# Optimization experiments

Hardware: AMD Instinct MI355X
Metric: run time of the kernel (lower is better)

## Reference

```python
import jax, jax.numpy as jnp
import numpy as np

B, S, D = 4, 2048, 512


def _dyt(x, alpha, w, b):
    return jnp.tanh(alpha * x) * w + b


def _fourier_fourier_attn(x, qr, qi, kr, ki, vr, vi, rtr, rti):
    xc = x.astype(jnp.complex64)
    qw, kw, vw, rtw = qr + 1j * qi, kr + 1j * ki, vr + 1j * vi, rtr + 1j * rti
    Xf = jnp.fft.fft(xc, axis=-1)  # [B,S,D] complex
    q = jnp.fft.fft(Xf * qw, axis=-2)
    k = jnp.fft.fft(Xf * kw, axis=-2)
    v = jnp.fft.fft(Xf * vw, axis=-2)
    rt = q / (k + 1e-12) * v
    rt = jnp.fft.ifft(rt, axis=-2) * rtw
    return jnp.fft.ifft(rt, axis=-1).real


def _fourier_sdpa(x, qr, qi, kr, ki, vr, vi):
    xc = x.astype(jnp.complex64)
    Xf = jnp.fft.fft(xc, axis=-1)
    proj = lambda w: jnp.fft.ifft(Xf * w, axis=-1).real
    q = proj(qr + 1j * qi)
    k = proj(kr + 1j * ki)
    v = proj(vr + 1j * vi)
    scores = jnp.einsum('bsd,btd->bst', q, k) / np.sqrt(D).astype(np.float32)
    attn = jax.nn.softmax(scores, axis=-1)
    return jnp.einsum('bst,btd->bsd', attn, v)


def _fourier_ffn(x, ar, ai, br, bi, bias):
    # Faithful to the source: the gelu branch is overwritten (dead code),
    # the returned value only uses the b-weighted FFT path.
    xc = x.astype(jnp.complex64)
    Xf = jnp.fft.fft(xc, axis=-1)
    h = jnp.fft.ifft(Xf * (ar + 1j * ai), axis=-1).real + bias
    h = jax.nn.gelu(h, approximate=False)  # discarded, as in the original
    return jnp.fft.ifft(Xf * (br + 1j * bi), axis=-1).real


def setup_inputs() -> dict:
    key = jax.random.key(0)
    ks = jax.random.split(key, 32)
    d = {'x': jax.random.normal(ks[0], (B, S, D), dtype=jnp.float32)}
    names_real = ['a_qr', 'a_kr', 'a_vr', 'a_rtr', 'b_qr', 'b_kr', 'b_vr', 'f_ar', 'f_br']
    names_imag = ['a_qi', 'a_ki', 'a_vi', 'a_rti', 'b_qi', 'b_ki', 'b_vi', 'f_ai', 'f_bi']
    i = 1
    for n in names_real:
        d[n] = 1.0 + 0.02 * jax.random.normal(ks[i], (D,), dtype=jnp.float32); i += 1
    for n in names_imag:
        d[n] = 0.02 * jax.random.normal(ks[i], (D,), dtype=jnp.float32); i += 1
    d['f_bias'] = 0.02 * jax.random.normal(ks[i], (D,), dtype=jnp.float32); i += 1
    for p in ['dyta', 'dytb', 'dytf']:
        d[p + '_alpha'] = jnp.full((1,), 0.5, dtype=jnp.float32)
        d[p + '_w'] = 1.0 + 0.02 * jax.random.normal(ks[i], (D,), dtype=jnp.float32); i += 1
        d[p + '_b'] = 0.02 * jax.random.normal(ks[i], (D,), dtype=jnp.float32); i += 1
    return d


def reference(x, a_qr, a_qi, a_kr, a_ki, a_vr, a_vi, a_rtr, a_rti,
              dyta_alpha, dyta_w, dyta_b,
              b_qr, b_qi, b_kr, b_ki, b_vr, b_vi,
              dytb_alpha, dytb_w, dytb_b,
              f_ar, f_ai, f_br, f_bi, f_bias,
              dytf_alpha, dytf_w, dytf_b):
    # attn_a block: FourierFourierAttention(DyT(x)) + x
    x = _fourier_fourier_attn(_dyt(x, dyta_alpha, dyta_w, dyta_b),
                              a_qr, a_qi, a_kr, a_ki, a_vr, a_vi, a_rtr, a_rti) + x
    # attn_b block: FourierScaledDotProductAttention(DyT(x)) + x
    x = _fourier_sdpa(_dyt(x, dytb_alpha, dytb_w, dytb_b),
                      b_qr, b_qi, b_kr, b_ki, b_vr, b_vi) + x
    # ffn block: FourierForwardNetwork(DyT(x)) + x
    x = _fourier_ffn(_dyt(x, dytf_alpha, dytf_w, dytf_b),
                     f_ar, f_ai, f_br, f_bi, f_bias) + x
    return x
```

## Files before the change

kernel.cpp:

```cpp
#include <hip/hip_runtime.h>


typedef __attribute__((ext_vector_type(8))) __bf16 bf16x8;
typedef __attribute__((ext_vector_type(4))) float floatx4;
typedef __attribute__((ext_vector_type(8))) _Float16 halfx8;
typedef __attribute__((ext_vector_type(8))) unsigned short ushortx8;
typedef __attribute__((ext_vector_type(2))) _Float16 half2v;
typedef __attribute__((ext_vector_type(4))) _Float16 half4v;

__device__ __forceinline__ unsigned short f2bf(float x) {
    unsigned u = __float_as_uint(x);
    u = (u + 0x7fffu + ((u >> 16) & 1u)) >> 16;
    return (unsigned short)u;
}

__device__ __forceinline__ float dyt_tanh(float x) {
    float e = __expf(2.0f * x);
    return 1.0f - 2.0f / (e + 1.0f);
}

__device__ __forceinline__ void async_load16(const unsigned short* g, unsigned short* l) {
    __builtin_amdgcn_global_load_lds(
        (const __attribute__((address_space(1))) unsigned int*)g,
        (__attribute__((address_space(3))) unsigned int*)l, 16, 0, 0);
}

__device__ __forceinline__ void wtw512(float (&tc)[12], float (&ts)[12], int lane) {
    const float w = -6.28318530717958647692f / 512.0f;
#pragma unroll
    for (int j = 0; j < 4; j++) __sincosf(w * (float)(j * 64 + lane), &ts[j], &tc[j]);
#pragma unroll
    for (int j = 0; j < 2; j++) __sincosf(w * (float)(2 * (j * 64 + lane)), &ts[4 + j], &tc[4 + j]);
    __sincosf(w * (float)(4 * lane), &ts[6], &tc[6]);
    __sincosf(w * (float)(8 * (lane & 31)), &ts[7], &tc[7]);
    __sincosf(w * (float)(16 * (lane & 15)), &ts[8], &tc[8]);
    __sincosf(w * (float)(32 * (lane & 7)), &ts[9], &tc[9]);
    __sincosf(w * (float)(64 * (lane & 3)), &ts[10], &tc[10]);
    __sincosf(w * (float)(128 * (lane & 1)), &ts[11], &tc[11]);
}

template <bool INV>
__device__ __forceinline__ void wfft512(float (&re)[8], float (&im)[8],
                                        const float (&tc)[12], const float (&ts)[12], int lane) {
    if (!INV) {
#pragma unroll
        for (int j = 0; j < 4; j++) {
            float ur = re[j], ui = im[j], vr = re[j + 4], vi = im[j + 4];
            re[j] = ur + vr; im[j] = ui + vi;
            float dr = ur - vr, di = ui - vi;
            re[j + 4] = dr * tc[j] - di * ts[j];
            im[j + 4] = dr * ts[j] + di * tc[j];
        }
#pragma unroll
        for (int g = 0; g < 8; g += 4)
#pragma unroll
            for (int jj = 0; jj < 2; jj++) {
                int j = g + jj;
                float ur = re[j], ui = im[j], vr = re[j + 2], vi = im[j + 2];
                re[j] = ur + vr; im[j] = ui + vi;
                float dr = ur - vr, di = ui - vi;
                re[j + 2] = dr * tc[4 + jj] - di * ts[4 + jj];
                im[j + 2] = dr * ts[4 + jj] + di * tc[4 + jj];
            }
#pragma unroll
        for (int j = 0; j < 8; j += 2) {
            float ur = re[j], ui = im[j], vr = re[j + 1], vi = im[j + 1];
            re[j] = ur + vr; im[j] = ui + vi;
            float dr = ur - vr, di = ui - vi;
            re[j + 1] = dr * tc[6] - di * ts[6];
            im[j + 1] = dr * ts[6] + di * tc[6];
        }
#pragma unroll
        for (int st = 0; st < 6; st++) {
            int h = 32 >> st;
            bool hi = (lane & h) != 0;
            float c = (st < 5) ? tc[7 + st] : 1.0f;
            float s = (st < 5) ? ts[7 + st] : 0.0f;
#pragma unroll
            for (int j = 0; j < 8; j++) {
                float orr = __shfl_xor(re[j], h, 64);
                float oii = __shfl_xor(im[j], h, 64);
                float dr = orr - re[j], di = oii - im[j];
                float sr = re[j] + orr, si = im[j] + oii;
                re[j] = hi ? (dr * c - di * s) : sr;
                im[j] = hi ? (dr * s + di * c) : si;
            }
        }
    } else {
#pragma unroll
        for (int st = 5; st >= 0; st--) {
            int h = 32 >> st;
            bool hi = (lane & h) != 0;
            float c = (st < 5) ? tc[7 + st] : 1.0f;
            float s = (st < 5) ? ts[7 + st] : 0.0f;
#pragma unroll
            for (int j = 0; j < 8; j++) {
                float zr = re[j], zi = im[j];
                float vr = zr * c + zi * s;
                float vi = zi * c - zr * s;
                float mr = hi ? vr : zr;
                float mi = hi ? vi : zi;
                float orr = __shfl_xor(mr, h, 64);
                float oii = __shfl_xor(mi, h, 64);
                re[j] = hi ? (orr - vr) : (zr + orr);
                im[j] = hi ? (oii - vi) : (zi + oii);
            }
        }
#pragma unroll
        for (int j = 0; j < 8; j += 2) {
            float vr = re[j + 1] * tc[6] + im[j + 1] * ts[6];
            float vi = im[j + 1] * tc[6] - re[j + 1] * ts[6];
            re[j + 1] = re[j] - vr; im[j + 1] = im[j] - vi;
            re[j] += vr; im[j] += vi;
        }
#pragma unroll
        for (int g = 0; g < 8; g += 4)
#pragma unroll
            for (int jj = 0; jj < 2; jj++) {
                int j = g + jj;
                float vr = re[j + 2] * tc[4 + jj] + im[j + 2] * ts[4 + jj];
                float vi = im[j + 2] * tc[4 + jj] - re[j + 2] * ts[4 + jj];
                re[j + 2] = re[j] - vr; im[j + 2] = im[j] - vi;
                re[j] += vr; im[j] += vi;
            }
#pragma unroll
        for (int j = 0; j < 4; j++) {
            float vr = re[j + 4] * tc[j] + im[j + 4] * ts[j];
            float vi = im[j + 4] * tc[j] - re[j + 4] * ts[j];
            re[j + 4] = re[j] - vr; im[j + 4] = im[j] - vi;
            re[j] += vr; im[j] += vi;
        }
    }
}

__global__ __launch_bounds__(256, 4) void k1_dyt_fftd(
        const float* __restrict__ x,
        const float* __restrict__ alpha, const float* __restrict__ w, const float* __restrict__ bia,
        half2v* __restrict__ xf) {
    int tid = threadIdx.x, lane = tid & 63, wv = tid >> 6;
    size_t row = (size_t)blockIdx.x * 4 + wv;
    float tc[12], ts[12];
    wtw512(tc, ts, lane);
    float re[8], im[8];
    float a = alpha[0];
    const float* xr = x + row * 512;
#pragma unroll
    for (int j = 0; j < 8; j++) {
        int d = j * 64 + lane;
        re[j] = dyt_tanh(a * xr[d]) * w[d] + bia[d];
        im[j] = 0.f;
    }
    wfft512<false>(re, im, tc, ts, lane);
#pragma unroll
    for (int j = 0; j < 8; j++) {
        int d = j * 64 + lane;
        xf[row * 512 + d] = (half2v){(_Float16)re[j], (_Float16)im[j]};
    }
}

__device__ __forceinline__ int pidx4(int i) { return i + (i >> 3); }

__device__ __forceinline__ void r4_fwd(float4* X, int t, int h, const half2v* tw) {
    int pos = t & (h - 1);
    int i = ((t & ~(h - 1)) << 2) | pos;
    int i0 = pidx4(i), i1 = pidx4(i + h), i2 = pidx4(i + 2 * h), i3 = pidx4(i + 3 * h);
    float4 a0 = X[i0], a1 = X[i1], a2 = X[i2], a3 = X[i3];
    half2v wv = tw[pos];
    float c1 = (float)wv.x, s1 = (float)wv.y;
    float c2 = c1 * c1 - s1 * s1, s2 = 2.f * c1 * s1;
    float c3 = c2 * c1 - s2 * s1, s3 = s2 * c1 + c2 * s1;
    float4 o0, o1, o2, o3;
    {
        float t0r = a0.x + a2.x, t0i = a0.y + a2.y, t1r = a0.x - a2.x, t1i = a0.y - a2.y;
        float t2r = a1.x + a3.x, t2i = a1.y + a3.y, t3r = a1.x - a3.x, t3i = a1.y - a3.y;
        o0.x = t0r + t2r; o0.y = t0i + t2i;
        float b1r = t1r + t3i, b1i = t1i - t3r;
        float b2r = t0r - t2r, b2i = t0i - t2i;
        float b3r = t1r - t3i, b3i = t1i + t3r;
        o1.x = b1r * c1 - b1i * s1; o1.y = b1r * s1 + b1i * c1;
        o2.x = b2r * c2 - b2i * s2; o2.y = b2r * s2 + b2i * c2;
        o3.x = b3r * c3 - b3i * s3; o3.y = b3r * s3 + b3i * c3;
    }
    {
        float t0r = a0.z + a2.z, t0i = a0.w + a2.w, t1r = a0.z - a2.z, t1i = a0.w - a2.w;
        float t2r = a1.z + a3.z, t2i = a1.w + a3.w, t3r = a1.z - a3.z, t3i = a1.w - a3.w;
        o0.z = t0r + t2r; o0.w = t0i + t2i;
        float b1r = t1r + t3i, b1i = t1i - t3r;
        float b2r = t0r - t2r, b2i = t0i - t2i;
        float b3r = t1r - t3i, b3i = t1i + t3r;
        o1.z = b1r * c1 - b1i * s1; o1.w = b1r * s1 + b1i * c1;
        o2.z = b2r * c2 - b2i * s2; o2.w = b2r * s2 + b2i * c2;
        o3.z = b3r * c3 - b3i * s3; o3.w = b3r * s3 + b3i * c3;
    }
    X[i0] = o0; X[i1] = o1; X[i2] = o2; X[i3] = o3;
}

__device__ __forceinline__ void r4_inv(float4* X, int t, int h, const half2v* tw) {
    int pos = t & (h - 1);
    int i = ((t & ~(h - 1)) << 2) | pos;
    int i0 = pidx4(i), i1 = pidx4(i + h), i2 = pidx4(i + 2 * h), i3 = pidx4(i + 3 * h);
    float4 y0 = X[i0], y1 = X[i1], y2 = X[i2], y3 = X[i3];
    half2v wv = tw[pos];
    float c1 = (float)wv.x, s1 = (float)wv.y;
    float c2 = c1 * c1 - s1 * s1, s2 = 2.f * c1 * s1;
    float c3 = c2 * c1 - s2 * s1, s3 = s2 * c1 + c2 * s1;
    float4 o0, o1, o2, o3;
    {
        float u1r = y1.x * c1 + y1.y * s1, u1i = y1.y * c1 - y1.x * s1;
        float u2r = y2.x * c2 + y2.y * s2, u2i = y2.y * c2 - y2.x * s2;
        float u3r = y3.x * c3 + y3.y * s3, u3i = y3.y * c3 - y3.x * s3;
        float s0r = y0.x + u2r, s0i = y0.y + u2i;
        float s1r = y0.x - u2r, s1i = y0.y - u2i;
        float s2r = u1r + u3r, s2i = u1i + u3i;
        float s3r = u1r - u3r, s3i = u1i - u3i;
        o0.x = s0r + s2r; o0.y = s0i + s2i;
        o2.x = s0r - s2r; o2.y = s0i - s2i;
        o1.x = s1r - s3i; o1.y = s1i + s3r;
        o3.x = s1r + s3i; o3.y = s1i - s3r;
    }
    {
        float u1r = y1.z * c1 + y1.w * s1, u1i = y1.w * c1 - y1.z * s1;
        float u2r = y2.z * c2 + y2.w * s2, u2i = y2.w * c2 - y2.z * s2;
        float u3r = y3.z * c3 + y3.w * s3, u3i = y3.w * c3 - y3.z * s3;
        float s0r = y0.z + u2r, s0i = y0.w + u2i;
        float s1r = y0.z - u2r, s1i = y0.w - u2i;
        float s2r = u1r + u3r, s2i = u1i + u3i;
        float s3r = u1r - u3r, s3i = u1i - u3i;
        o0.z = s0r + s2r; o0.w = s0i + s2i;
        o2.z = s0r - s2r; o2.w = s0i - s2i;
        o1.z = s1r - s3i; o1.w = s1i + s3r;
        o3.z = s1r + s3i; o3.w = s1i - s3r;
    }
    X[i0] = o0; X[i1] = o1; X[i2] = o2; X[i3] = o3;
}

__global__ __launch_bounds__(512) void k2_sfft(
        half2v* __restrict__ xf,
        const float* __restrict__ qr, const float* __restrict__ qi,
        const float* __restrict__ kr, const float* __restrict__ ki,
        const float* __restrict__ vr, const float* __restrict__ vi,
        const float* __restrict__ rtr, const float* __restrict__ rti) {
    __shared__ float4 buf[2304];
    __shared__ half2v twd[682];
    int t = threadIdx.x;
    int g = blockIdx.x;
    int xcd = g & 7, r = g >> 3;
    int pp = xcd * 32 + (r & 31);
    int b = r >> 5;
    int p0 = pp * 2;
    half4v* colh = (half4v*)(xf + (size_t)b * 2048 * 512 + p0);

    for (int i = t; i < 682; i += 512) {
        int h, off;
        if (i < 512)      { h = 512; off = 0; }
        else if (i < 640) { h = 128; off = 512; }
        else if (i < 672) { h = 32;  off = 640; }
        else if (i < 680) { h = 8;   off = 672; }
        else              { h = 2;   off = 680; }
        int pos = i - off;
        float s, c;
        __sincosf(-6.28318530717958647692f * (float)pos / (float)(4 * h), &s, &c);
        twd[i] = (half2v){(_Float16)c, (_Float16)s};
    }

#pragma unroll
    for (int c = 0; c < 4; c++) {
        int s = t + 512 * c;
        half4v h = colh[(size_t)s * 256];
        buf[pidx4(s)] = make_float4((float)h.x, (float)h.y, (float)h.z, (float)h.w);
    }
    __syncthreads(); r4_fwd(buf, t, 512, twd);
    __syncthreads(); r4_fwd(buf, t, 128, twd + 512);
    __syncthreads(); r4_fwd(buf, t, 32, twd + 640);
    __syncthreads(); r4_fwd(buf, t, 8, twd + 672);
    __syncthreads(); r4_fwd(buf, t, 2, twd + 680);
    __syncthreads();
#pragma unroll
    for (int c = 0; c < 2; c++) {
        int pr = t + 512 * c;
        int ia = pidx4(2 * pr), ib = pidx4(2 * pr + 1);
        float4 a = buf[ia], bb = buf[ib];
        buf[ia] = make_float4(a.x + bb.x, a.y + bb.y, a.z + bb.z, a.w + bb.w);
        buf[ib] = make_float4(a.x - bb.x, a.y - bb.y, a.z - bb.z, a.w - bb.w);
    }
    __syncthreads();

    int f0 = __brev((unsigned)p0) >> 23;
    int f1 = __brev((unsigned)(p0 + 1)) >> 23;
    float qw0r = qr[f0], qw0i = qi[f0], kw0r = kr[f0], kw0i = ki[f0], vw0r = vr[f0], vw0i = vi[f0];
    float qw1r = qr[f1], qw1i = qi[f1], kw1r = kr[f1], kw1i = ki[f1], vw1r = vr[f1], vw1i = vi[f1];
#pragma unroll
    for (int c = 0; c < 4; c++) {
        int idx = pidx4(t + 512 * c);
        float4 y = buf[idx];
        {
            float yr = y.x, yi = y.y;
            float qre = yr * qw0r - yi * qw0i, qim = yr * qw0i + yi * qw0r;
            float kre = yr * kw0r - yi * kw0i + 1e-12f, kim = yr * kw0i + yi * kw0r;
            float vre = yr * vw0r - yi * vw0i, vim = yr * vw0i + yi * vw0r;
            float inv = 1.0f / (kre * kre + kim * kim);
            float dre = (qre * kre + qim * kim) * inv;
            float dim = (qim * kre - qre * kim) * inv;
            y.x = dre * vre - dim * vim;
            y.y = dre * vim + dim * vre;
        }
        {
            float yr = y.z, yi = y.w;
            float qre = yr * qw1r - yi * qw1i, qim = yr * qw1i + yi * qw1r;
            float kre = yr * kw1r - yi * kw1i + 1e-12f, kim = yr * kw1i + yi * kw1r;
            float vre = yr * vw1r - yi * vw1i, vim = yr * vw1i + yi * vw1r;
            float inv = 1.0f / (kre * kre + kim * kim);
            float dre = (qre * kre + qim * kim) * inv;
            float dim = (qim * kre - qre * kim) * inv;
            y.z = dre * vre - dim * vim;
            y.w = dre * vim + dim * vre;
        }
        buf[idx] = y;
    }

    __syncthreads();
#pragma unroll
    for (int c = 0; c < 2; c++) {
        int pr = t + 512 * c;
        int ia = pidx4(2 * pr), ib = pidx4(2 * pr + 1);
        float4 a = buf[ia], bb = buf[ib];
        buf[ia] = make_float4(a.x + bb.x, a.y + bb.y, a.z + bb.z, a.w + bb.w);
        buf[ib] = make_float4(a.x - bb.x, a.y - bb.y, a.z - bb.z, a.w - bb.w);
    }
    __syncthreads(); r4_inv(buf, t, 2, twd + 680);
    __syncthreads(); r4_inv(buf, t, 8, twd + 672);
    __syncthreads(); r4_inv(buf, t, 32, twd + 640);
    __syncthreads(); r4_inv(buf, t, 128, twd + 512);
    __syncthreads(); r4_inv(buf, t, 512, twd);
    __syncthreads();

    const float sc = 1.0f / 2048.0f;
    float r0r = rtr[f0] * sc, r0i = rti[f0] * sc;
    float r1r = rtr[f1] * sc, r1i = rti[f1] * sc;
#pragma unroll
    for (int c = 0; c < 4; c++) {
        int s = t + 512 * c;
        float4 z = buf[pidx4(s)];
        float ox = z.x * r0r - z.y * r0i, oy = z.x * r0i + z.y * r0r;
        float oz = z.z * r1r - z.w * r1i, ow = z.z * r1i + z.w * r1r;
        colh[(size_t)s * 256] = (half4v){(_Float16)ox, (_Float16)oy, (_Float16)oz, (_Float16)ow};
    }
}

__global__ __launch_bounds__(256, 4) void k3_mid(
        const half2v* __restrict__ xf,
        const float* __restrict__ x,
        const float* __restrict__ alpha, const float* __restrict__ w, const float* __restrict__ bia,
        const float* __restrict__ qr, const float* __restrict__ qi,
        const float* __restrict__ kr, const float* __restrict__ ki,
        const float* __restrict__ vr, const float* __restrict__ vi,
        float* __restrict__ x1,
        unsigned short* __restrict__ qb, unsigned short* __restrict__ kb, unsigned short* __restrict__ vb) {
    __shared__ __align__(16) char smem[4 * 1024 * 8];
    int tid = threadIdx.x, lane = tid & 63, wv = tid >> 6;
    float2* zb = (float2*)(smem + wv * 8192);
    float* wbs = (float*)smem;
    float2* zf = (float2*)(smem + 12288 + wv * 4096);
    size_t pr = (size_t)blockIdx.x * 4 + wv;
    size_t r1 = pr * 2, r2 = r1 + 1;
    float tc[12], ts[12];
    wtw512(tc, ts, lane);

    float xa[8], xb2[8];
#pragma unroll
    for (int j = 0; j < 8; j++) {
        int d = j * 64 + lane;
        half2v h1 = xf[r1 * 512 + d];
        half2v h2 = xf[r2 * 512 + d];
        zb[d]       = make_float2((float)h1.x, (float)h1.y);
        zb[512 + d] = make_float2((float)h2.x, (float)h2.y);
        xa[j]  = x[r1 * 512 + d];
        xb2[j] = x[r2 * 512 + d];
    }
    float re[8], im[8];
#pragma unroll
    for (int j = 0; j < 8; j++) {
        int d = j * 64 + lane;
        int fd = __brev((unsigned)d) >> 23;
        int dp = __brev((unsigned)((512 - fd) & 511)) >> 23;
        float2 z1 = zb[d], z1p = zb[dp];
        float2 z2 = zb[512 + d], z2p = zb[512 + dp];
        float h1r = 0.5f * (z1.x + z1p.x), h1i = 0.5f * (z1.y - z1p.y);
        float h2r = 0.5f * (z2.x + z2p.x), h2i = 0.5f * (z2.y - z2p.y);
        re[j] = h1r - h2i;
        im[j] = h1i + h2r;
    }
    __syncthreads();
    for (int idx = tid; idx < 512; idx += 256) {
        int f = __brev((unsigned)idx) >> 23;
        int gg = (512 - f) & 511;
        float aa = (f == 0 || f == 256) ? 0.04419417382415922f : 0.0625f;
        float ah = aa * 0.5f;
        const float s5 = 0.5f * (1.0f / 512.0f);
        wbs[0 * 512 + idx] = ah * (qr[f] + qr[gg]); wbs[1 * 512 + idx] = ah * (qi[f] - qi[gg]);
        wbs[2 * 512 + idx] = ah * (kr[f] + kr[gg]); wbs[3 * 512 + idx] = ah * (ki[f] - ki[gg]);
        wbs[4 * 512 + idx] = s5 * (vr[f] + vr[gg]); wbs[5 * 512 + idx] = s5 * (vi[f] - vi[gg]);
    }

    wfft512<true>(re, im, tc, ts, lane);
    float a = alpha[0];
    float gre[8], gim[8];
#pragma unroll
    for (int j = 0; j < 8; j++) {
        int d = j * 64 + lane;
        float v1 = re[j] * (1.0f / 512.0f) + xa[j];
        float v2 = im[j] * (1.0f / 512.0f) + xb2[j];
        x1[r1 * 512 + d] = v1;
        x1[r2 * 512 + d] = v2;
        gre[j] = dyt_tanh(a * v1) * w[d] + bia[d];
        gim[j] = dyt_tanh(a * v2) * w[d] + bia[d];
    }
    wfft512<false>(gre, gim, tc, ts, lane);
    __syncthreads();

#pragma unroll
    for (int j = 0; j < 8; j++)
        zf[j * 64 + lane] = make_float2(gre[j], gim[j]);

    float pvr[8], pvi[8];
#pragma unroll
    for (int j = 0; j < 8; j++) {
        int i = j * 64 + lane;
        float wr0 = wbs[4 * 512 + i], wi0 = wbs[5 * 512 + i];
        pvr[j] = gre[j] * wr0 - gim[j] * wi0;
        pvi[j] = gre[j] * wi0 + gim[j] * wr0;
    }

    bool odd = (lane & 1) != 0;
#pragma unroll
    for (int j = 0; j < 8; j++) {
        int d = j * 64 + lane;
        int fd = __brev((unsigned)d) >> 23;
        int dp = __brev((unsigned)((512 - fd) & 511)) >> 23;
        float2 Zp = zf[dp];
        float zr = gre[j], zi = gim[j];
        float A1r = 0.5f * (zr + Zp.x), A1i = 0.5f * (zi - Zp.y);
        float A2r = 0.5f * (zi + Zp.y), A2i = 0.5f * (Zp.x - zr);
        float wr0 = wbs[0 * 512 + d], wi0 = wbs[1 * 512 + d];
        float Q1r = A1r * wr0 - A1i * wi0, Q1i = A1r * wi0 + A1i * wr0;
        float Q2r = A2r * wr0 - A2i * wi0, Q2i = A2r * wi0 + A2i * wr0;
        qb[r1 * 512 + d] = f2bf(odd ? -Q1i : Q1r);
        qb[r2 * 512 + d] = f2bf(odd ? -Q2i : Q2r);
        float wr1 = wbs[2 * 512 + d], wi1 = wbs[3 * 512 + d];
        float K1r = A1r * wr1 - A1i * wi1, K1i = A1r * wi1 + A1i * wr1;
        float K2r = A2r * wr1 - A2i * wi1, K2i = A2r * wi1 + A2i * wr1;
        kb[r1 * 512 + d] = f2bf(odd ? -K1i : K1r);
        kb[r2 * 512 + d] = f2bf(odd ? -K2i : K2r);
    }

    wfft512<true>(pvr, pvi, tc, ts, lane);
#pragma unroll
    for (int j = 0; j < 8; j++) {
        int d = j * 64 + lane;
        vb[r1 * 512 + d] = f2bf(pvr[j]);
        vb[r2 * 512 + d] = f2bf(pvi[j]);
    }
}

__global__ __launch_bounds__(256) void gemm_bt(
        const unsigned short* __restrict__ A, const unsigned short* __restrict__ Bt,
        void* __restrict__ C, int M, int N, int Ks, int kseg, float scale, int out_half) {
    int tilesM = M >> 7, tilesN = N >> 7;
    int perBatch = tilesM * tilesN;
    int l = blockIdx.x;
    int seg = blockIdx.y;
    int s = l & 7, t = l >> 3;
    int cnt = perBatch >> 3;
    int bz = t / cnt;
    int u = t - bz * cnt;
    int pn = tilesN >> 1, pm = tilesM >> 2;
    int n0 = ((s & 1) * pn + (u % pn)) << 7;
    int m0 = ((s >> 1) * pm + (u / pn)) << 7;
    int kbase = seg * kseg;

    const unsigned short* Ab = A + (size_t)bz * M * Ks;
    const unsigned short* Bb = Bt + (size_t)bz * N * Ks;
    __shared__ __align__(16) unsigned short smem[2 * 128 * 64];
    unsigned short* As = smem;
    unsigned short* Bs = smem + 128 * 64;
    int tid = threadIdx.x;
    int wave = tid >> 6, lane = tid & 63;
    int wm = (wave >> 1) * 64, wn = (wave & 1) * 64;
    int lrow = lane & 15, lq = lane >> 4;
    floatx4 acc[4][4];
#pragma unroll
    for (int i = 0; i < 4; i++)
#pragma unroll
        for (int j = 0; j < 4; j++)
            acc[i][j] = (floatx4){0.f, 0.f, 0.f, 0.f};

    int lr = lane >> 3;
    int lcs = lane & 7;
    for (int k0 = kbase; k0 < kbase + kseg; k0 += 64) {
        __syncthreads();
#pragma unroll
        for (int i = 0; i < 4; i++) {
            int c = wave * 4 + i;
            int r = c * 8 + lr;
            int gcol = ((lcs ^ (r & 7)) << 3);
            async_load16(Ab + (size_t)(m0 + r) * Ks + k0 + gcol, As + c * 512);
            async_load16(Bb + (size_t)(n0 + r) * Ks + k0 + gcol, Bs + c * 512);
        }
        __syncthreads();
        bf16x8 a0[4], a1[4], b0[4], b1[4];
#pragma unroll
        for (int mi = 0; mi < 4; mi++) {
            int r = wm + mi * 16 + lrow;
            a0[mi] = *(const bf16x8*)(As + r * 64 + ((lq ^ (r & 7)) << 3));
            a1[mi] = *(const bf16x8*)(As + r * 64 + (((lq + 4) ^ (r & 7)) << 3));
        }
#pragma unroll
        for (int ni = 0; ni < 4; ni++) {
            int r = wn + ni * 16 + lrow;
            b0[ni] = *(const bf16x8*)(Bs + r * 64 + ((lq ^ (r & 7)) << 3));
            b1[ni] = *(const bf16x8*)(Bs + r * 64 + (((lq + 4) ^ (r & 7)) << 3));
        }
#pragma unroll
        for (int mi = 0; mi < 4; mi++)
#pragma unroll
            for (int ni = 0; ni < 4; ni++) {
                acc[mi][ni] = __builtin_amdgcn_mfma_f32_16x16x32_bf16(a0[mi], b0[ni], acc[mi][ni], 0, 0, 0);
                acc[mi][ni] = __builtin_amdgcn_mfma_f32_16x16x32_bf16(a1[mi], b1[ni], acc[mi][ni], 0, 0, 0);
            }
    }
    size_t cbase = ((size_t)seg * 4 + bz) * (size_t)M * N;
    int lr0 = (wave >> 1) * 16 + lq * 4;
    for (int mi = 0; mi < 4; mi++) {
        __syncthreads();
        if (out_half) {
            _Float16* Cs = (_Float16*)smem;
            for (int ni = 0; ni < 4; ni++)
                for (int r = 0; r < 4; r++)
                    Cs[(lr0 + r) * 128 + wn + ni * 16 + lrow] = (_Float16)(acc[mi][ni][r] * scale);
            __syncthreads();
            for (int h = 0; h < 2; h++) {
                int chunk = tid + h * 256;
                int rl = chunk >> 4, cb = (chunk & 15) * 16;
                int grow = m0 + mi * 16 + (rl & 15) + (rl >> 4) * 64;
                *(uint4*)((char*)C + (cbase + (size_t)grow * N + n0) * 2 + cb) =
                    *(const uint4*)((const char*)Cs + rl * 256 + cb);
            }
        } else {
            float* Cs = (float*)smem;
            for (int ni = 0; ni < 4; ni++)
                for (int r = 0; r < 4; r++)
                    Cs[(lr0 + r) * 128 + wn + ni * 16 + lrow] = acc[mi][ni][r] * scale;
            __syncthreads();
            for (int h = 0; h < 4; h++) {
                int chunk = tid + h * 256;
                int rl = chunk >> 5, cb = (chunk & 31) * 16;
                int grow = m0 + mi * 16 + (rl & 15) + (rl >> 4) * 64;
                *(uint4*)((char*)C + (cbase + (size_t)grow * N + n0) * 4 + cb) =
                    *(const uint4*)((const char*)Cs + rl * 512 + cb);
            }
        }
    }
}

__global__ __launch_bounds__(256) void sm_tr(
        const _Float16* __restrict__ Sc, unsigned short* __restrict__ P,
        const unsigned short* __restrict__ vb, unsigned short* __restrict__ vT) {
    __shared__ __align__(16) char lds[64 * 65 * 2];
    if (blockIdx.x < 8192) {
        float* red = (float*)lds;
        int tid = threadIdx.x;
        size_t row = blockIdx.x;
        halfx8 hv = *(const halfx8*)(Sc + row * 2048 + tid * 8);
        float v[8];
#pragma unroll
        for (int j = 0; j < 8; j++) v[j] = (float)hv[j];
        float mx = v[0];
#pragma unroll
        for (int j = 1; j < 8; j++) mx = fmaxf(mx, v[j]);
        for (int off = 32; off >= 1; off >>= 1) mx = fmaxf(mx, __shfl_xor(mx, off));
        int wv = tid >> 6;
        if ((tid & 63) == 0) red[wv] = mx;
        __syncthreads();
        mx = fmaxf(fmaxf(red[0], red[1]), fmaxf(red[2], red[3]));
        float e[8], sum = 0.f;
#pragma unroll
        for (int j = 0; j < 8; j++) { e[j] = __expf(v[j] - mx); sum += e[j]; }
        for (int off = 32; off >= 1; off >>= 1) sum += __shfl_xor(sum, off);
        __syncthreads();
        if ((tid & 63) == 0) red[wv] = sum;
        __syncthreads();
        float inv = 1.0f / (red[0] + red[1] + red[2] + red[3]);
        ushortx8 o;
#pragma unroll
        for (int j = 0; j < 8; j++) o[j] = f2bf(e[j] * inv);
        *(ushortx8*)(P + row * 2048 + tid * 8) = o;
    } else {
        unsigned short (*tile)[65] = (unsigned short (*)[65])lds;
        int id = blockIdx.x - 8192;
        int sx = id & 31, dy = (id >> 5) & 7, bz = id >> 8;
        int s0 = sx * 64, d0 = dy * 64;
        int tx = threadIdx.x & 63, ty = threadIdx.x >> 6;
        for (int j = 0; j < 16; j++) {
            int s = ty + j * 4;
            tile[s][tx] = vb[((size_t)bz * 2048 + s0 + s) * 512 + d0 + tx];
        }
        __syncthreads();
        for (int j = 0; j < 16; j++) {
            int d = ty + j * 4;
            vT[((size_t)bz * 512 + d0 + d) * 2048 + s0 + tx] = tile[tx][d];
        }
    }
}

__global__ __launch_bounds__(256, 4) void k5_ffn(
        const _Float16* __restrict__ attn0, const _Float16* __restrict__ attn1,
        const float* __restrict__ x1,
        const float* __restrict__ alpha, const float* __restrict__ w, const float* __restrict__ bia,
        const float* __restrict__ br, const float* __restrict__ bi,
        float* __restrict__ out) {
    __shared__ float wbs[2][512];
    int tid = threadIdx.x, lane = tid & 63, wv = tid >> 6;
    size_t pr = (size_t)blockIdx.x * 4 + wv;
    size_t r1 = pr * 2, r2 = r1 + 1;
    for (int idx = tid; idx < 512; idx += 256) {
        int f = __brev((unsigned)idx) >> 23;
        int gg = (512 - f) & 511;
        wbs[0][idx] = 0.5f * (br[f] + br[gg]) * (1.0f / 512.0f);
        wbs[1][idx] = 0.5f * (bi[f] - bi[gg]) * (1.0f / 512.0f);
    }
    float tc[12], ts[12];
    wtw512(tc, ts, lane);
    float a = alpha[0];
    float re[8], im[8], x2a[8], x2b[8];
#pragma unroll
    for (int j = 0; j < 8; j++) {
        int d = j * 64 + lane;
        float v1 = (float)attn0[r1 * 512 + d] + (float)attn1[r1 * 512 + d] + x1[r1 * 512 + d];
        float v2 = (float)attn0[r2 * 512 + d] + (float)attn1[r2 * 512 + d] + x1[r2 * 512 + d];
        x2a[j] = v1; x2b[j] = v2;
        re[j] = dyt_tanh(a * v1) * w[d] + bia[d];
        im[j] = dyt_tanh(a * v2) * w[d] + bia[d];
    }
    wfft512<false>(re, im, tc, ts, lane);
    __syncthreads();
#pragma unroll
    for (int j = 0; j < 8; j++) {
        int i = j * 64 + lane;
        float wr0 = wbs[0][i], wi0 = wbs[1][i];
        float rr = re[j], ii = im[j];
        re[j] = rr * wr0 - ii * wi0;
        im[j] = rr * wi0 + ii * wr0;
    }
    wfft512<true>(re, im, tc, ts, lane);
#pragma unroll
    for (int j = 0; j < 8; j++) {
        int d = j * 64 + lane;
        out[r1 * 512 + d] = re[j] + x2a[j];
        out[r2 * 512 + d] = im[j] + x2b[j];
    }
}

extern "C" void kernel_launch(void* const* d_in, const int* in_sizes, int n_in,
                              void* d_out, int out_size, void* d_ws, size_t ws_size,
                              hipStream_t stream) {
    const float* x      = (const float*)d_in[0];
    const float* a_qr   = (const float*)d_in[1];
    const float* a_kr   = (const float*)d_in[2];
    const float* a_vr   = (const float*)d_in[3];
    const float* a_rtr  = (const float*)d_in[4];
    const float* b_qr   = (const float*)d_in[5];
    const float* b_kr   = (const float*)d_in[6];
    const float* b_vr   = (const float*)d_in[7];
    const float* f_br   = (const float*)d_in[9];
    const float* a_qi   = (const float*)d_in[10];
    const float* a_ki   = (const float*)d_in[11];
    const float* a_vi   = (const float*)d_in[12];
    const float* a_rti  = (const float*)d_in[13];
    const float* b_qi   = (const float*)d_in[14];
    const float* b_ki   = (const float*)d_in[15];
    const float* b_vi   = (const float*)d_in[16];
    const float* f_bi   = (const float*)d_in[18];
    const float* dyta_alpha = (const float*)d_in[20];
    const float* dyta_w     = (const float*)d_in[21];
    const float* dyta_b     = (const float*)d_in[22];
    const float* dytb_alpha = (const float*)d_in[23];
    const float* dytb_w     = (const float*)d_in[24];
    const float* dytb_b     = (const float*)d_in[25];
    const float* dytf_alpha = (const float*)d_in[26];
    const float* dytf_w     = (const float*)d_in[27];
    const float* dytf_b     = (const float*)d_in[28];
    (void)in_sizes; (void)n_in; (void)out_size; (void)ws_size;

    char* ws = (char*)d_ws;
    const size_t MB = 1024 * 1024;
    half2v* xfH = (half2v*)(ws + 0 * MB);
    float* x1   = (float*)(ws + 32 * MB);
    unsigned short* qb = (unsigned short*)(ws + 48 * MB);
    unsigned short* kb = (unsigned short*)(ws + 56 * MB);
    unsigned short* vb = (unsigned short*)(ws + 64 * MB);
    unsigned short* vT = (unsigned short*)(ws + 72 * MB);
    _Float16* scores   = (_Float16*)(ws + 0 * MB);
    unsigned short* Pb = (unsigned short*)(ws + 0 * MB);
    _Float16* attnP    = (_Float16*)(ws + 81 * MB);
    float* outp = (float*)d_out;

    k1_dyt_fftd<<<2048, 256, 0, stream>>>(x, dyta_alpha, dyta_w, dyta_b, xfH);
    k2_sfft<<<1024, 512, 0, stream>>>(xfH, a_qr, a_qi, a_kr, a_ki, a_vr, a_vi, a_rtr, a_rti);
    k3_mid<<<1024, 256, 0, stream>>>(xfH, x, dytb_alpha, dytb_w, dytb_b,
                                     b_qr, b_qi, b_kr, b_ki, b_vr, b_vi, x1, qb, kb, vb);
    gemm_bt<<<1024, 256, 0, stream>>>(qb, kb, scores, 2048, 2048, 512, 512,
                                      0.04419417382415922f, 1);
    sm_tr<<<9216, 256, 0, stream>>>(scores, Pb, vb, vT);
    gemm_bt<<<dim3(256, 2), 256, 0, stream>>>(Pb, vT, attnP, 2048, 512, 2048, 1024,
                                              1.0f, 1);
    k5_ffn<<<1024, 256, 0, stream>>>(attnP, attnP + (size_t)4 * 2048 * 512, x1,
                                     dytf_alpha, dytf_w, dytf_b, f_br, f_bi, outp);
}
```

Baseline: 279.9 us.

## Process four rows per wave in k3_mid with a dual interleaved FFT

```diff
diff --git a/kernel.cpp b/kernel.cpp
--- a/kernel.cpp
+++ b/kernel.cpp
@@ -129,6 +129,171 @@
             float vi = im[j + 4] * tc[j] - re[j + 4] * ts[j];
             re[j + 4] = re[j] - vr; im[j + 4] = im[j] - vi;
             re[j] += vr; im[j] += vi;
+        }
+    }
+}
+
+template <bool INV>
+__device__ __forceinline__ void wfft512d(float (&reA)[8], float (&imA)[8],
+                                         float (&reB)[8], float (&imB)[8],
+                                         const float (&tc)[12], const float (&ts)[12], int lane) {
+    if (!INV) {
+#pragma unroll
+        for (int j = 0; j < 4; j++) {
+            {
+                float ur = reA[j], ui = imA[j], vr = reA[j + 4], vi = imA[j + 4];
+                reA[j] = ur + vr; imA[j] = ui + vi;
+                float dr = ur - vr, di = ui - vi;
+                reA[j + 4] = dr * tc[j] - di * ts[j];
+                imA[j + 4] = dr * ts[j] + di * tc[j];
+            }
+            {
+                float ur = reB[j], ui = imB[j], vr = reB[j + 4], vi = imB[j + 4];
+                reB[j] = ur + vr; imB[j] = ui + vi;
+                float dr = ur - vr, di = ui - vi;
+                reB[j + 4] = dr * tc[j] - di * ts[j];
+                imB[j + 4] = dr * ts[j] + di * tc[j];
+            }
+        }
+#pragma unroll
+        for (int g = 0; g < 8; g += 4)
+#pragma unroll
+            for (int jj = 0; jj < 2; jj++) {
+                int j = g + jj;
+                {
+                    float ur = reA[j], ui = imA[j], vr = reA[j + 2], vi = imA[j + 2];
+                    reA[j] = ur + vr; imA[j] = ui + vi;
+                    float dr = ur - vr, di = ui - vi;
+                    reA[j + 2] = dr * tc[4 + jj] - di * ts[4 + jj];
+                    imA[j + 2] = dr * ts[4 + jj] + di * tc[4 + jj];
+                }
+                {
+                    float ur = reB[j], ui = imB[j], vr = reB[j + 2], vi = imB[j + 2];
+                    reB[j] = ur + vr; imB[j] = ui + vi;
+                    float dr = ur - vr, di = ui - vi;
+                    reB[j + 2] = dr * tc[4 + jj] - di * ts[4 + jj];
+                    imB[j + 2] = dr * ts[4 + jj] + di * tc[4 + jj];
+                }
+            }
+#pragma unroll
+        for (int j = 0; j < 8; j += 2) {
+            {
+                float ur = reA[j], ui = imA[j], vr = reA[j + 1], vi = imA[j + 1];
+                reA[j] = ur + vr; imA[j] = ui + vi;
+                float dr = ur - vr, di = ui - vi;
+                reA[j + 1] = dr * tc[6] - di * ts[6];
+                imA[j + 1] = dr * ts[6] + di * tc[6];
+            }
+            {
+                float ur = reB[j], ui = imB[j], vr = reB[j + 1], vi = imB[j + 1];
+                reB[j] = ur + vr; imB[j] = ui + vi;
+                float dr = ur - vr, di = ui - vi;
+                reB[j + 1] = dr * tc[6] - di * ts[6];
+                imB[j + 1] = dr * ts[6] + di * tc[6];
+            }
+        }
+#pragma unroll
+        for (int st = 0; st < 6; st++) {
+            int h = 32 >> st;
+            bool hi = (lane & h) != 0;
+            float c = (st < 5) ? tc[7 + st] : 1.0f;
+            float s = (st < 5) ? ts[7 + st] : 0.0f;
+#pragma unroll
+            for (int j = 0; j < 8; j++) {
+                float oAr = __shfl_xor(reA[j], h, 64);
+                float oAi = __shfl_xor(imA[j], h, 64);
+                float oBr = __shfl_xor(reB[j], h, 64);
+                float oBi = __shfl_xor(imB[j], h, 64);
+                {
+                    float dr = oAr - reA[j], di = oAi - imA[j];
+                    float sr = reA[j] + oAr, si = imA[j] + oAi;
+                    reA[j] = hi ? (dr * c - di * s) : sr;
+                    imA[j] = hi ? (dr * s + di * c) : si;
+                }
+                {
+                    float dr = oBr - reB[j], di = oBi - imB[j];
+                    float sr = reB[j] + oBr, si = imB[j] + oBi;
+                    reB[j] = hi ? (dr * c - di * s) : sr;
+                    imB[j] = hi ? (dr * s + di * c) : si;
+                }
+            }
+        }
+    } else {
+#pragma unroll
+        for (int st = 5; st >= 0; st--) {
+            int h = 32 >> st;
+            bool hi = (lane & h) != 0;
+            float c = (st < 5) ? tc[7 + st] : 1.0f;
+            float s = (st < 5) ? ts[7 + st] : 0.0f;
+#pragma unroll
+            for (int j = 0; j < 8; j++) {
+                float zAr = reA[j], zAi = imA[j];
+                float vAr = zAr * c + zAi * s;
+                float vAi = zAi * c - zAr * s;
+                float mAr = hi ? vAr : zAr;
+                float mAi = hi ? vAi : zAi;
+                float zBr = reB[j], zBi = imB[j];
+                float vBr = zBr * c + zBi * s;
+                float vBi = zBi * c - zBr * s;
+                float mBr = hi ? vBr : zBr;
+                float mBi = hi ? vBi : zBi;
+                float oAr = __shfl_xor(mAr, h, 64);
+                float oAi = __shfl_xor(mAi, h, 64);
+                float oBr = __shfl_xor(mBr, h, 64);
+                float oBi = __shfl_xor(mBi, h, 64);
+                reA[j] = hi ? (oAr - vAr) : (zAr + oAr);
+                imA[j] = hi ? (oAi - vAi) : (zAi + oAi);
+                reB[j] = hi ? (oBr - vBr) : (zBr + oBr);
+                imB[j] = hi ? (oBi - vBi) : (zBi + oBi);
+            }
+        }
+#pragma unroll
+        for (int j = 0; j < 8; j += 2) {
+            {
+                float vr = reA[j + 1] * tc[6] + imA[j + 1] * ts[6];
+                float vi = imA[j + 1] * tc[6] - reA[j + 1] * ts[6];
+                reA[j + 1] = reA[j] - vr; imA[j + 1] = imA[j] - vi;
+                reA[j] += vr; imA[j] += vi;
+            }
+            {
+                float vr = reB[j + 1] * tc[6] + imB[j + 1] * ts[6];
+                float vi = imB[j + 1] * tc[6] - reB[j + 1] * ts[6];
+                reB[j + 1] = reB[j] - vr; imB[j + 1] = imB[j] - vi;
+                reB[j] += vr; imB[j] += vi;
+            }
+        }
+#pragma unroll
+        for (int g = 0; g < 8; g += 4)
+#pragma unroll
+            for (int jj = 0; jj < 2; jj++) {
+                int j = g + jj;
+                {
+                    float vr = reA[j + 2] * tc[4 + jj] + imA[j + 2] * ts[4 + jj];
+                    float vi = imA[j + 2] * tc[4 + jj] - reA[j + 2] * ts[4 + jj];
+                    reA[j + 2] = reA[j] - vr; imA[j + 2] = imA[j] - vi;
+                    reA[j] += vr; imA[j] += vi;
+                }
+                {
+                    float vr = reB[j + 2] * tc[4 + jj] + imB[j + 2] * ts[4 + jj];
+                    float vi = imB[j + 2] * tc[4 + jj] - reB[j + 2] * ts[4 + jj];
+                    reB[j + 2] = reB[j] - vr; imB[j + 2] = imB[j] - vi;
+                    reB[j] += vr; imB[j] += vi;
+                }
+            }
+#pragma unroll
+        for (int j = 0; j < 4; j++) {
+            {
+                float vr = reA[j + 4] * tc[j] + imA[j + 4] * ts[j];
+                float vi = imA[j + 4] * tc[j] - reA[j + 4] * ts[j];
+                reA[j + 4] = reA[j] - vr; imA[j + 4] = imA[j] - vi;
+                reA[j] += vr; imA[j] += vi;
+            }
+            {
+                float vr = reB[j + 4] * tc[j] + imB[j + 4] * ts[j];
+                float vi = imB[j + 4] * tc[j] - reB[j + 4] * ts[j];
+                reB[j + 4] = reB[j] - vr; imB[j + 4] = imB[j] - vi;
+                reB[j] += vr; imB[j] += vi;
+            }
         }
     }
 }
@@ -347,7 +512,7 @@
     }
 }
 
-__global__ __launch_bounds__(256, 4) void k3_mid(
+__global__ __launch_bounds__(256, 2) void k3_mid(
         const half2v* __restrict__ xf,
         const float* __restrict__ x,
         const float* __restrict__ alpha, const float* __restrict__ w, const float* __restrict__ bia,
@@ -361,23 +526,23 @@
     float2* zb = (float2*)(smem + wv * 8192);
     float* wbs = (float*)smem;
     float2* zf = (float2*)(smem + 12288 + wv * 4096);
-    size_t pr = (size_t)blockIdx.x * 4 + wv;
-    size_t r1 = pr * 2, r2 = r1 + 1;
+    size_t wid = (size_t)blockIdx.x * 4 + wv;
+    size_t r1A = wid * 4, r2A = r1A + 1, r1B = r1A + 2, r2B = r1A + 3;
     float tc[12], ts[12];
     wtw512(tc, ts, lane);
 
-    float xa[8], xb2[8];
-#pragma unroll
-    for (int j = 0; j < 8; j++) {
-        int d = j * 64 + lane;
-        half2v h1 = xf[r1 * 512 + d];
-        half2v h2 = xf[r2 * 512 + d];
+    float xaA[8], xbA[8], xaB[8], xbB[8];
+    float reA[8], imA[8], reB[8], imB[8];
+#pragma unroll
+    for (int j = 0; j < 8; j++) {
+        int d = j * 64 + lane;
+        half2v h1 = xf[r1A * 512 + d];
+        half2v h2 = xf[r2A * 512 + d];
         zb[d]       = make_float2((float)h1.x, (float)h1.y);
         zb[512 + d] = make_float2((float)h2.x, (float)h2.y);
-        xa[j]  = x[r1 * 512 + d];
-        xb2[j] = x[r2 * 512 + d];
-    }
-    float re[8], im[8];
+        xaA[j] = x[r1A * 512 + d];
+        xbA[j] = x[r2A * 512 + d];
+    }
 #pragma unroll
     for (int j = 0; j < 8; j++) {
         int d = j * 64 + lane;
@@ -387,8 +552,30 @@
         float2 z2 = zb[512 + d], z2p = zb[512 + dp];
         float h1r = 0.5f * (z1.x + z1p.x), h1i = 0.5f * (z1.y - z1p.y);
         float h2r = 0.5f * (z2.x + z2p.x), h2i = 0.5f * (z2.y - z2p.y);
-        re[j] = h1r - h2i;
-        im[j] = h1i + h2r;
+        reA[j] = h1r - h2i;
+        imA[j] = h1i + h2r;
+    }
+#pragma unroll
+    for (int j = 0; j < 8; j++) {
+        int d = j * 64 + lane;
+        half2v h1 = xf[r1B * 512 + d];
+        half2v h2 = xf[r2B * 512 + d];
+        zb[d]       = make_float2((float)h1.x, (float)h1.y);
+        zb[512 + d] = make_float2((float)h2.x, (float)h2.y);
+        xaB[j] = x[r1B * 512 + d];
+        xbB[j] = x[r2B * 512 + d];
+    }
+#pragma unroll
+    for (int j = 0; j < 8; j++) {
+        int d = j * 64 + lane;
+        int fd = __brev((unsigned)d) >> 23;
+        int dp = __brev((unsigned)((512 - fd) & 511)) >> 23;
+        float2 z1 = zb[d], z1p = zb[dp];
+        float2 z2 = zb[512 + d], z2p = zb[512 + dp];
+        float h1r = 0.5f * (z1.x + z1p.x), h1i = 0.5f * (z1.y - z1p.y);
+        float h2r = 0.5f * (z2.x + z2p.x), h2i = 0.5f * (z2.y - z2p.y);
+        reB[j] = h1r - h2i;
+        imB[j] = h1i + h2r;
     }
     __syncthreads();
     for (int idx = tid; idx < 512; idx += 256) {
@@ -402,63 +589,103 @@
         wbs[4 * 512 + idx] = s5 * (vr[f] + vr[gg]); wbs[5 * 512 + idx] = s5 * (vi[f] - vi[gg]);
     }
 
-    wfft512<true>(re, im, tc, ts, lane);
+    wfft512d<true>(reA, imA, reB, imB, tc, ts, lane);
     float a = alpha[0];
-    float gre[8], gim[8];
-#pragma unroll
-    for (int j = 0; j < 8; j++) {
-        int d = j * 64 + lane;
-        float v1 = re[j] * (1.0f / 512.0f) + xa[j];
-        float v2 = im[j] * (1.0f / 512.0f) + xb2[j];
-        x1[r1 * 512 + d] = v1;
-        x1[r2 * 512 + d] = v2;
-        gre[j] = dyt_tanh(a * v1) * w[d] + bia[d];
-        gim[j] = dyt_tanh(a * v2) * w[d] + bia[d];
-    }
-    wfft512<false>(gre, gim, tc, ts, lane);
+    float greA[8], gimA[8], greB[8], gimB[8];
+#pragma unroll
+    for (int j = 0; j < 8; j++) {
+        int d = j * 64 + lane;
+        float v1 = reA[j] * (1.0f / 512.0f) + xaA[j];
+        float v2 = imA[j] * (1.0f / 512.0f) + xbA[j];
+        x1[r1A * 512 + d] = v1;
+        x1[r2A * 512 + d] = v2;
+        greA[j] = dyt_tanh(a * v1) * w[d] + bia[d];
+        gimA[j] = dyt_tanh(a * v2) * w[d] + bia[d];
+    }
+#pragma unroll
+    for (int j = 0; j < 8; j++) {
+        int d = j * 64 + lane;
+        float v1 = reB[j] * (1.0f / 512.0f) + xaB[j];
+        float v2 = imB[j] * (1.0f / 512.0f) + xbB[j];
+        x1[r1B * 512 + d] = v1;
+        x1[r2B * 512 + d] = v2;
+        greB[j] = dyt_tanh(a * v1) * w[d] + bia[d];
+        gimB[j] = dyt_tanh(a * v2) * w[d] + bia[d];
+    }
+    wfft512d<false>(greA, gimA, greB, gimB, tc, ts, lane);
     __syncthreads();
 
+    bool odd = (lane & 1) != 0;
+    float pvrA[8], pviA[8], pvrB[8], pviB[8];
 #pragma unroll
     for (int j = 0; j < 8; j++)
-        zf[j * 64 + lane] = make_float2(gre[j], gim[j]);
-
-    float pvr[8], pvi[8];
+        zf[j * 64 + lane] = make_float2(greA[j], gimA[j]);
 #pragma unroll
     for (int j = 0; j < 8; j++) {
         int i = j * 64 + lane;
         float wr0 = wbs[4 * 512 + i], wi0 = wbs[5 * 512 + i];
-        pvr[j] = gre[j] * wr0 - gim[j] * wi0;
-        pvi[j] = gre[j] * wi0 + gim[j] * wr0;
-    }
-
-    bool odd = (lane & 1) != 0;
+        pvrA[j] = greA[j] * wr0 - gimA[j] * wi0;
+        pviA[j] = greA[j] * wi0 + gimA[j] * wr0;
+    }
 #pragma unroll
     for (int j = 0; j < 8; j++) {
         int d = j * 64 + lane;
         int fd = __brev((unsigned)d) >> 23;
         int dp = __brev((unsigned)((512 - fd) & 511)) >> 23;
         float2 Zp = zf[dp];
-        float zr = gre[j], zi = gim[j];
+        float zr = greA[j], zi = gimA[j];
         float A1r = 0.5f * (zr + Zp.x), A1i = 0.5f * (zi - Zp.y);
         float A2r = 0.5f * (zi + Zp.y), A2i = 0.5f * (Zp.x - zr);
         float wr0 = wbs[0 * 512 + d], wi0 = wbs[1 * 512 + d];
         float Q1r = A1r * wr0 - A1i * wi0, Q1i = A1r * wi0 + A1i * wr0;
         float Q2r = A2r * wr0 - A2i * wi0, Q2i = A2r * wi0 + A2i * wr0;
-        qb[r1 * 512 + d] = f2bf(odd ? -Q1i : Q1r);
-        qb[r2 * 512 + d] = f2bf(odd ? -Q2i : Q2r);
+        qb[r1A * 512 + d] = f2bf(odd ? -Q1i : Q1r);
+        qb[r2A * 512 + d] = f2bf(odd ? -Q2i : Q2r);
         float wr1 = wbs[2 * 512 + d], wi1 = wbs[3 * 512 + d];
         float K1r = A1r * wr1 - A1i * wi1, K1i = A1r * wi1 + A1i * wr1;
         float K2r = A2r * wr1 - A2i * wi1, K2i = A2r * wi1 + A2i * wr1;
-        kb[r1 * 512 + d] = f2bf(odd ? -K1i : K1r);
-        kb[r2 * 512 + d] = f2bf(odd ? -K2i : K2r);
-    }
-
-    wfft512<true>(pvr, pvi, tc, ts, lane);
-#pragma unroll
-    for (int j = 0; j < 8; j++) {
-        int d = j * 64 + lane;
-        vb[r1 * 512 + d] = f2bf(pvr[j]);
-        vb[r2 * 512 + d] = f2bf(pvi[j]);
+        kb[r1A * 512 + d] = f2bf(odd ? -K1i : K1r);
+        kb[r2A * 512 + d] = f2bf(odd ? -K2i : K2r);
+    }
+#pragma unroll
+    for (int j = 0; j < 8; j++)
+        zf[j * 64 + lane] = make_float2(greB[j], gimB[j]);
+#pragma unroll
+    for (int j = 0; j < 8; j++) {
+        int i = j * 64 + lane;
+        float wr0 = wbs[4 * 512 + i], wi0 = wbs[5 * 512 + i];
+        pvrB[j] = greB[j] * wr0 - gimB[j] * wi0;
+        pviB[j] = greB[j] * wi0 + gimB[j] * wr0;
+    }
+#pragma unroll
+    for (int j = 0; j < 8; j++) {
+        int d = j * 64 + lane;
+        int fd = __brev((unsigned)d) >> 23;
+        int dp = __brev((unsigned)((512 - fd) & 511)) >> 23;
+        float2 Zp = zf[dp];
+        float zr = greB[j], zi = gimB[j];
+        float A1r = 0.5f * (zr + Zp.x), A1i = 0.5f * (zi - Zp.y);
+        float A2r = 0.5f * (zi + Zp.y), A2i = 0.5f * (Zp.x - zr);
+        float wr0 = wbs[0 * 512 + d], wi0 = wbs[1 * 512 + d];
+        float Q1r = A1r * wr0 - A1i * wi0, Q1i = A1r * wi0 + A1i * wr0;
+        float Q2r = A2r * wr0 - A2i * wi0, Q2i = A2r * wi0 + A2i * wr0;
+        qb[r1B * 512 + d] = f2bf(odd ? -Q1i : Q1r);
+        qb[r2B * 512 + d] = f2bf(odd ? -Q2i : Q2r);
+        float wr1 = wbs[2 * 512 + d], wi1 = wbs[3 * 512 + d];
+        float K1r = A1r * wr1 - A1i * wi1, K1i = A1r * wi1 + A1i * wr1;
+        float K2r = A2r * wr1 - A2i * wi1, K2i = A2r * wi1 + A2i * wr1;
+        kb[r1B * 512 + d] = f2bf(odd ? -K1i : K1r);
+        kb[r2B * 512 + d] = f2bf(odd ? -K2i : K2r);
+    }
+
+    wfft512d<true>(pvrA, pviA, pvrB, pviB, tc, ts, lane);
+#pragma unroll
+    for (int j = 0; j < 8; j++) {
+        int d = j * 64 + lane;
+        vb[r1A * 512 + d] = f2bf(pvrA[j]);
+        vb[r2A * 512 + d] = f2bf(pviA[j]);
+        vb[r1B * 512 + d] = f2bf(pvrB[j]);
+        vb[r2B * 512 + d] = f2bf(pviB[j]);
     }
 }
 
@@ -706,8 +933,8 @@
 
     k1_dyt_fftd<<<2048, 256, 0, stream>>>(x, dyta_alpha, dyta_w, dyta_b, xfH);
     k2_sfft<<<1024, 512, 0, stream>>>(xfH, a_qr, a_qi, a_kr, a_ki, a_vr, a_vi, a_rtr, a_rti);
-    k3_mid<<<1024, 256, 0, stream>>>(xfH, x, dytb_alpha, dytb_w, dytb_b,
-                                     b_qr, b_qi, b_kr, b_ki, b_vr, b_vi, x1, qb, kb, vb);
+    k3_mid<<<512, 256, 0, stream>>>(xfH, x, dytb_alpha, dytb_w, dytb_b,
+                                    b_qr, b_qi, b_kr, b_ki, b_vr, b_vi, x1, qb, kb, vb);
     gemm_bt<<<1024, 256, 0, stream>>>(qb, kb, scores, 2048, 2048, 512, 512,
                                       0.04419417382415922f, 1);
     sm_tr<<<9216, 256, 0, stream>>>(scores, Pb, vb, vT);
```

New measurement: 384.6 us. 1.37x slower.
